# Optimization experiments

Hardware: AMD Instinct MI355X
Metric: run time of the kernel (lower is better)

## Reference

```python
import jax, jax.numpy as jnp
import numpy as np

EMB = 768
HEADS = 12
HEAD_DIM = EMB // HEADS  # 64
SCALE = 1.0 / float(np.sqrt(EMB))  # NOTE: source divides by sqrt(emb_size), not sqrt(head_dim)


def setup_inputs() -> dict:
    key = jax.random.key(0)
    k_x, k_wqkv, k_bqkv, k_wp, k_bp = jax.random.split(key, 5)
    b, n = 4, 2048
    x = jax.random.normal(k_x, (b, n, EMB), dtype=jnp.float32)
    # torch Linear default init ~ U(-1/sqrt(in), 1/sqrt(in)); scale doesn't matter for correctness baseline
    lim = 1.0 / np.sqrt(EMB)
    W_qkv = jax.random.uniform(k_wqkv, (EMB, 3 * EMB), minval=-lim, maxval=lim, dtype=jnp.float32)
    b_qkv = jax.random.uniform(k_bqkv, (3 * EMB,), minval=-lim, maxval=lim, dtype=jnp.float32)
    W_proj = jax.random.uniform(k_wp, (EMB, EMB), minval=-lim, maxval=lim, dtype=jnp.float32)
    b_proj = jax.random.uniform(k_bp, (EMB,), minval=-lim, maxval=lim, dtype=jnp.float32)
    return {"x": x, "W_qkv": W_qkv, "b_qkv": b_qkv, "W_proj": W_proj, "b_proj": b_proj}


def reference(x, W_qkv, b_qkv, W_proj, b_proj):
    b, n, _ = x.shape
    qkv = x @ W_qkv + b_qkv                              # [b, n, 3*emb]
    # rearrange 'b n (h d qkv) -> qkv b h n d' : qkv is the innermost split
    qkv = qkv.reshape(b, n, HEADS, HEAD_DIM, 3)
    qkv = jnp.transpose(qkv, (4, 0, 2, 1, 3))            # [3, b, h, n, d]
    q, k, v = qkv[0], qkv[1], qkv[2]
    att = jnp.einsum('bhnd,bhmd->bhnm', q, k) * SCALE    # [b, h, n, n]
    att = jax.nn.softmax(att, axis=-1)
    # dropout is identity at inference
    out = jnp.einsum('bhnm,bhmd->bhnd', att, v)          # [b, h, n, d]
    out = jnp.transpose(out, (0, 2, 1, 3)).reshape(b, n, EMB)  # 'b h n d -> b n (h d)'
    return out @ W_proj + b_proj
```

## Files before the change

### kernel.cpp

```cpp
#include <hip/hip_runtime.h>
#include <math.h>

typedef _Float16 f16x8 __attribute__((ext_vector_type(8)));
typedef _Float16 f16x4 __attribute__((ext_vector_type(4)));
typedef float f32x4 __attribute__((ext_vector_type(4)));
typedef unsigned int uint32;
typedef unsigned short ushort16;

static constexpr int EMB_ = 768;
static constexpr int NH_ = 12;
static constexpr int HD_ = 64;
static constexpr int SEQ_ = 2048;
static constexpr int B_ = 4;
static constexpr float QSCALE_ = 0.036084391824351615f * 1.4426950408889634f;

__device__ __forceinline__ void gload_lds16(const void* g, void* l) {
    __builtin_amdgcn_global_load_lds((const __attribute__((address_space(1))) void*)g,
                                     (__attribute__((address_space(3))) void*)l,
                                     16, 0, 0);
}

__global__ __launch_bounds__(256)
void prep_k(const float* __restrict__ W0, _Float16* __restrict__ Wt0,
            const float* __restrict__ W1, _Float16* __restrict__ Wt1,
            const float* __restrict__ x, _Float16* __restrict__ xh,
            int C0, int C1, int n4)
{
    const int tid = threadIdx.x;
    if (blockIdx.z == 2) {
        const int stride = 72 * 24 * 256;
        for (int i = (blockIdx.y * 72 + blockIdx.x) * 256 + tid; i < n4; i += stride) {
            float4 v = ((const float4*)x)[i];
            f16x4 o = {(_Float16)v.x, (_Float16)v.y, (_Float16)v.z, (_Float16)v.w};
            ((f16x4*)xh)[i] = o;
        }
        return;
    }
    const float* W; _Float16* Wt; int C;
    if (blockIdx.z == 0) { W = W0; Wt = Wt0; C = C0; }
    else                 { W = W1; Wt = Wt1; C = C1; }
    const int c0 = blockIdx.x * 32;
    if (c0 >= C) return;
    const int r0 = blockIdx.y * 32;
    __shared__ float ls[32][33];
    const int tc = tid & 31, tr = tid >> 5;
#pragma unroll
    for (int i = 0; i < 4; ++i)
        ls[tr + 8 * i][tc] = W[(size_t)(r0 + tr + 8 * i) * C + c0 + tc];
    __syncthreads();
#pragma unroll
    for (int i = 0; i < 4; ++i)
        Wt[(size_t)(c0 + tr + 8 * i) * EMB_ + r0 + tc] = (_Float16)ls[tc][tr + 8 * i];
}

template<int EPI>
__global__ __launch_bounds__(256, 2)
void gemm16(const _Float16* __restrict__ A, const _Float16* __restrict__ Bt,
            const float* __restrict__ bias, float* __restrict__ outF,
            _Float16* __restrict__ hq, _Float16* __restrict__ hk,
            _Float16* __restrict__ hv,
            int M, int N, int K)
{
    __shared__ __align__(16) _Float16 As[128 * 64];
    __shared__ __align__(16) _Float16 Bs[128 * 64];

    const int tid  = threadIdx.x;
    const int lane = tid & 63;
    const int w    = tid >> 6;
    const int txm  = lane & 15, g = lane >> 4;
    const int wr   = w >> 1, wc = w & 1;
    const int m0   = blockIdx.y * 128, n0 = blockIdx.x * 128;
    const int nk   = K >> 6;

    const int sr  = lane >> 3;
    const int scX = (((lane & 7) ^ sr) << 3);
    const _Float16* gA[4]; const _Float16* gB[4];
    _Float16* lA[4]; _Float16* lB[4];
#pragma unroll
    for (int i = 0; i < 4; ++i) {
        const int row = w * 32 + 8 * i;
        gA[i] = A  + (size_t)(m0 + row + sr) * K + scX;
        gB[i] = Bt + (size_t)(n0 + row + sr) * K + scX;
        lA[i] = As + row * 64 + lane * 8;
        lB[i] = Bs + row * 64 + lane * 8;
    }

    f32x4 acc[4][4];
#pragma unroll
    for (int i = 0; i < 4; ++i)
#pragma unroll
        for (int j = 0; j < 4; ++j) acc[i][j] = (f32x4){0.f, 0.f, 0.f, 0.f};

    const int fsw = txm & 7;

    for (int kt = 0; kt < nk; ++kt) {
        __syncthreads();
#pragma unroll
        for (int i = 0; i < 4; ++i) gload_lds16(gA[i] + kt * 64, lA[i]);
#pragma unroll
        for (int i = 0; i < 4; ++i) gload_lds16(gB[i] + kt * 64, lB[i]);
        __syncthreads();

#pragma unroll
        for (int kh = 0; kh < 2; ++kh) {
            const int coff = ((4 * kh + g) ^ fsw) << 3;
            f16x8 af[4], bf[4];
#pragma unroll
            for (int i = 0; i < 4; ++i)
                af[i] = *(const f16x8*)&As[(wr * 64 + 16 * i + txm) * 64 + coff];
#pragma unroll
            for (int j = 0; j < 4; ++j)
                bf[j] = *(const f16x8*)&Bs[(wc * 64 + 16 * j + txm) * 64 + coff];
#pragma unroll
            for (int i = 0; i < 4; ++i)
#pragma unroll
                for (int j = 0; j < 4; ++j)
                    acc[i][j] = __builtin_amdgcn_mfma_f32_16x16x32_f16(af[i], bf[j], acc[i][j], 0, 0, 0);
        }
    }

    if (EPI == 0) {
#pragma unroll
        for (int i = 0; i < 4; ++i) {
            const int mB = m0 + wr * 64 + 16 * i + 4 * g;
#pragma unroll
            for (int j = 0; j < 4; ++j) {
                const int n = n0 + wc * 64 + 16 * j + txm;
                const float bv = bias[n];
                const int h   = n / 192;
                const int rem = n - h * 192;
                const int dd  = rem / 3;
                const int s   = rem - dd * 3;
                _Float16* bse = (s == 0) ? hq : (s == 1) ? hk : hv;
                const float scl = (s == 0) ? QSCALE_ : 1.f;
#pragma unroll
                for (int r = 0; r < 4; ++r) {
                    const int mm = mB + r;
                    const int bb = mm >> 11;
                    const int nn = mm & (SEQ_ - 1);
                    const int ddE = (s == 1) ? (dd ^ ((nn & 7) * 8)) : dd;
                    bse[(((size_t)(bb * NH_ + h)) * SEQ_ + nn) * HD_ + ddE] =
                        (_Float16)((acc[i][j][r] + bv) * scl);
                }
            }
        }
    } else {
#pragma unroll
        for (int i = 0; i < 4; ++i) {
#pragma unroll
            for (int r = 0; r < 4; ++r) {
                const int mm = m0 + wr * 64 + 16 * i + 4 * g + r;
                float* dst = outF + (size_t)mm * N + n0 + wc * 64 + txm;
#pragma unroll
                for (int j = 0; j < 4; ++j)
                    dst[16 * j] = acc[i][j][r] + bias[n0 + wc * 64 + 16 * j + txm];
            }
        }
    }
}

__global__ __launch_bounds__(256, 3)
void attn_k(const _Float16* __restrict__ Qb, const _Float16* __restrict__ Kb,
            const _Float16* __restrict__ Vb, _Float16* __restrict__ Out)
{
    __shared__ __align__(16) _Float16 Ks[2][64][64];
    __shared__ __align__(16) _Float16 Vs[2][64][72];

    const int tid  = threadIdx.x;
    const int lane = tid & 63;
    const int wv   = tid >> 6;
    const int txm  = lane & 15;
    const int g    = lane >> 4;

    const int lin  = blockIdx.x;
    const int slot = lin >> 3;
    const int bh   = (lin & 7) + 8 * (slot >> 4);
    const int q0   = (slot & 15) << 7;
    const int bb   = bh / NH_;
    const int hh   = bh - bb * NH_;

    const _Float16* KpB = Kb + (size_t)bh * SEQ_ * HD_;
    const _Float16* VpB = Vb + (size_t)bh * SEQ_ * HD_;

    auto kstage = [&](int buf, int kt) {
        const int c0 = kt << 6;
#pragma unroll
        for (int i = 0; i < 2; ++i)
            gload_lds16(KpB + (size_t)(c0 + 16 * wv + 8 * i) * HD_ + lane * 8,
                        &Ks[buf][16 * wv + 8 * i][0] + lane * 8);
    };
    kstage(0, 0);

    f16x8 qf[2][2];
#pragma unroll
    for (int s = 0; s < 2; ++s)
#pragma unroll
        for (int kh = 0; kh < 2; ++kh)
            qf[s][kh] = *(const f16x8*)(Qb +
                ((size_t)bh * SEQ_ + q0 + 32 * wv + 16 * s + txm) * HD_ + 32 * kh + 8 * g);

    const int vc = (tid & 31) << 1;
    const int vd = (tid >> 5) << 3;
    const int swz = (txm & 7) * 8;

    f32x4 o[2][4];
#pragma unroll
    for (int s = 0; s < 2; ++s)
#pragma unroll
        for (int dt = 0; dt < 4; ++dt) o[s][dt] = (f32x4){0.f, 0.f, 0.f, 0.f};
    float li[2] = {0.f, 0.f};

    uint4 va = *(const uint4*)(VpB + (size_t)vc * HD_ + vd);
    uint4 vb = *(const uint4*)(VpB + (size_t)(vc + 1) * HD_ + vd);

    constexpr int NT = SEQ_ / 64;
    for (int kt = 0; kt < NT; ++kt) {
        const int buf = kt & 1;
        {
            const ushort16* pa = (const ushort16*)&va;
            const ushort16* pb = (const ushort16*)&vb;
#pragma unroll
            for (int j = 0; j < 8; ++j) {
                uint32 wrd = (uint32)pa[j] | ((uint32)pb[j] << 16);
                *(uint32*)&Vs[buf][vd + j][vc] = wrd;
            }
        }
        __syncthreads();

        if (kt + 1 < NT) {
            kstage(buf ^ 1, kt + 1);
            const int c0n = (kt + 1) << 6;
            va = *(const uint4*)(VpB + (size_t)(c0n + vc) * HD_ + vd);
            vb = *(const uint4*)(VpB + (size_t)(c0n + vc + 1) * HD_ + vd);
        }

        f16x8 kf[4][2];
#pragma unroll
        for (int ct = 0; ct < 4; ++ct)
#pragma unroll
            for (int kh = 0; kh < 2; ++kh)
                kf[ct][kh] = *(const f16x8*)&Ks[buf][16 * ct + txm][(32 * kh + 8 * g) ^ swz];

        f32x4 st[2][4];
#pragma unroll
        for (int s = 0; s < 2; ++s)
#pragma unroll
            for (int ct = 0; ct < 4; ++ct) {
                f32x4 a = (f32x4){0.f, 0.f, 0.f, 0.f};
                a = __builtin_amdgcn_mfma_f32_16x16x32_f16(kf[ct][0], qf[s][0], a, 0, 0, 0);
                a = __builtin_amdgcn_mfma_f32_16x16x32_f16(kf[ct][1], qf[s][1], a, 0, 0, 0);
                st[s][ct] = a;
            }

        f16x4 vf[4][4];
#pragma unroll
        for (int dt = 0; dt < 4; ++dt)
#pragma unroll
            for (int ct = 0; ct < 4; ++ct)
                vf[dt][ct] = *(const f16x4*)&Vs[buf][16 * dt + txm][16 * ct + 4 * g];

#pragma unroll
        for (int s = 0; s < 2; ++s) {
            f16x4 pb4[4];
#pragma unroll
            for (int ct = 0; ct < 4; ++ct) {
                float p0 = __builtin_amdgcn_exp2f(st[s][ct][0]);
                float p1 = __builtin_amdgcn_exp2f(st[s][ct][1]);
                float p2 = __builtin_amdgcn_exp2f(st[s][ct][2]);
                float p3 = __builtin_amdgcn_exp2f(st[s][ct][3]);
                li[s] += (p0 + p1) + (p2 + p3);
                pb4[ct] = (f16x4){(_Float16)p0, (_Float16)p1, (_Float16)p2, (_Float16)p3};
            }
#pragma unroll
            for (int dt = 0; dt < 4; ++dt) {
                f32x4 a = o[s][dt];
#pragma unroll
                for (int ct = 0; ct < 4; ++ct)
                    a = __builtin_amdgcn_mfma_f32_16x16x16f16(vf[dt][ct], pb4[ct], a, 0, 0, 0);
                o[s][dt] = a;
            }
        }
    }

#pragma unroll
    for (int s = 0; s < 2; ++s) {
        float rs = li[s];
        rs += __shfl_xor(rs, 16);
        rs += __shfl_xor(rs, 32);
        const float inv = 1.f / rs;
        const int q = q0 + 32 * wv + 16 * s + txm;
        _Float16* dst = Out + ((size_t)bb * SEQ_ + q) * EMB_ + hh * HD_;
#pragma unroll
        for (int dt = 0; dt < 4; ++dt) {
            f16x4 pk = {(_Float16)(o[s][dt][0] * inv), (_Float16)(o[s][dt][1] * inv),
                        (_Float16)(o[s][dt][2] * inv), (_Float16)(o[s][dt][3] * inv)};
            *(f16x4*)(dst + 16 * dt + 4 * g) = pk;
        }
    }
}

extern "C" void kernel_launch(void* const* d_in, const int* in_sizes, int n_in,
                              void* d_out, int out_size, void* d_ws, size_t ws_size,
                              hipStream_t stream)
{
    const float* x    = (const float*)d_in[0];
    const float* Wqkv = (const float*)d_in[1];
    const float* bqkv = (const float*)d_in[2];
    const float* Wp   = (const float*)d_in[3];
    const float* bp   = (const float*)d_in[4];
    float* out = (float*)d_out;

    const size_t PER = (size_t)B_ * NH_ * SEQ_ * HD_;
    _Float16* Qh     = (_Float16*)d_ws;
    _Float16* Kh     = Qh + PER;
    _Float16* Vh     = Kh + PER;
    _Float16* xh     = Vh + PER;
    _Float16* WqkvT  = xh + (size_t)B_ * SEQ_ * EMB_;
    _Float16* WprojT = WqkvT + (size_t)EMB_ * 3 * EMB_;
    _Float16* Ah     = WprojT + (size_t)EMB_ * EMB_;

    const int M = B_ * SEQ_;

    prep_k<<<dim3(72, 24, 3), dim3(256), 0, stream>>>(
        Wqkv, WqkvT, Wp, WprojT, x, xh, 3 * EMB_, EMB_, B_ * SEQ_ * EMB_ / 4);

    gemm16<0><<<dim3(3 * EMB_ / 128, M / 128), dim3(256), 0, stream>>>(
        xh, WqkvT, bqkv, nullptr, Qh, Kh, Vh, M, 3 * EMB_, EMB_);

    attn_k<<<dim3((SEQ_ / 128) * B_ * NH_), dim3(256), 0, stream>>>(Qh, Kh, Vh, Ah);

    gemm16<1><<<dim3(EMB_ / 128, M / 128), dim3(256), 0, stream>>>(
        Ah, WprojT, bp, out, nullptr, nullptr, nullptr, M, EMB_, EMB_);
}
```

Before: 233.0 us.

## Double-buffer GEMM LDS tiles and remap blocks to a grouped 1D grid

The fp16 GEMM kernel now keeps two LDS buffers per operand and issues the global-to-LDS loads for the next K tile before computing on the current one. This removes one barrier per iteration and lets load latency overlap with the MFMA work. The launch also becomes a 1D grid whose block index is remapped so groups of 8 consecutive blocks share an N tile across adjacent M tiles, which is meant to improve L2 reuse of the weight operand. LDS use per block doubles to 64 KB, which could limit occupancy. Only the QKV and output-projection GEMMs change; the attention kernel, which is likely the larger share of runtime, is untouched.

```diff
diff --git a/kernel.cpp b/kernel.cpp
--- a/kernel.cpp
+++ b/kernel.cpp
@@ -61,29 +61,40 @@
             _Float16* __restrict__ hv,
             int M, int N, int K)
 {
-    __shared__ __align__(16) _Float16 As[128 * 64];
-    __shared__ __align__(16) _Float16 Bs[128 * 64];
+    __shared__ __align__(16) _Float16 As[2][128 * 64];
+    __shared__ __align__(16) _Float16 Bs[2][128 * 64];
 
     const int tid  = threadIdx.x;
     const int lane = tid & 63;
     const int w    = tid >> 6;
     const int txm  = lane & 15, g = lane >> 4;
     const int wr   = w >> 1, wc = w & 1;
-    const int m0   = blockIdx.y * 128, n0 = blockIdx.x * 128;
+
+    const int lin  = blockIdx.x;
+    const int slot = lin >> 3;
+    const int mt   = (lin & 7) + 8 * (slot & 7);
+    const int nt   = slot >> 3;
+    const int m0   = mt * 128, n0 = nt * 128;
     const int nk   = K >> 6;
 
     const int sr  = lane >> 3;
     const int scX = (((lane & 7) ^ sr) << 3);
     const _Float16* gA[4]; const _Float16* gB[4];
-    _Float16* lA[4]; _Float16* lB[4];
 #pragma unroll
     for (int i = 0; i < 4; ++i) {
         const int row = w * 32 + 8 * i;
         gA[i] = A  + (size_t)(m0 + row + sr) * K + scX;
         gB[i] = Bt + (size_t)(n0 + row + sr) * K + scX;
-        lA[i] = As + row * 64 + lane * 8;
-        lB[i] = Bs + row * 64 + lane * 8;
-    }
+    }
+
+    auto stage = [&](int buf, int kt) {
+#pragma unroll
+        for (int i = 0; i < 4; ++i) {
+            const int row = w * 32 + 8 * i;
+            gload_lds16(gA[i] + kt * 64, &As[buf][row * 64] + lane * 8);
+            gload_lds16(gB[i] + kt * 64, &Bs[buf][row * 64] + lane * 8);
+        }
+    };
 
     f32x4 acc[4][4];
 #pragma unroll
@@ -93,13 +104,12 @@
 
     const int fsw = txm & 7;
 
+    stage(0, 0);
+
     for (int kt = 0; kt < nk; ++kt) {
+        const int buf = kt & 1;
         __syncthreads();
-#pragma unroll
-        for (int i = 0; i < 4; ++i) gload_lds16(gA[i] + kt * 64, lA[i]);
-#pragma unroll
-        for (int i = 0; i < 4; ++i) gload_lds16(gB[i] + kt * 64, lB[i]);
-        __syncthreads();
+        if (kt + 1 < nk) stage(buf ^ 1, kt + 1);
 
 #pragma unroll
         for (int kh = 0; kh < 2; ++kh) {
@@ -107,10 +117,10 @@
             f16x8 af[4], bf[4];
 #pragma unroll
             for (int i = 0; i < 4; ++i)
-                af[i] = *(const f16x8*)&As[(wr * 64 + 16 * i + txm) * 64 + coff];
+                af[i] = *(const f16x8*)&As[buf][(wr * 64 + 16 * i + txm) * 64 + coff];
 #pragma unroll
             for (int j = 0; j < 4; ++j)
-                bf[j] = *(const f16x8*)&Bs[(wc * 64 + 16 * j + txm) * 64 + coff];
+                bf[j] = *(const f16x8*)&Bs[buf][(wc * 64 + 16 * j + txm) * 64 + coff];
 #pragma unroll
             for (int i = 0; i < 4; ++i)
 #pragma unroll
@@ -324,11 +334,11 @@
     prep_k<<<dim3(72, 24, 3), dim3(256), 0, stream>>>(
         Wqkv, WqkvT, Wp, WprojT, x, xh, 3 * EMB_, EMB_, B_ * SEQ_ * EMB_ / 4);
 
-    gemm16<0><<<dim3(3 * EMB_ / 128, M / 128), dim3(256), 0, stream>>>(
+    gemm16<0><<<dim3((M / 128) * (3 * EMB_ / 128)), dim3(256), 0, stream>>>(
         xh, WqkvT, bqkv, nullptr, Qh, Kh, Vh, M, 3 * EMB_, EMB_);
 
     attn_k<<<dim3((SEQ_ / 128) * B_ * NH_), dim3(256), 0, stream>>>(Qh, Kh, Vh, Ah);
 
-    gemm16<1><<<dim3(EMB_ / 128, M / 128), dim3(256), 0, stream>>>(
+    gemm16<1><<<dim3((M / 128) * (EMB_ / 128)), dim3(256), 0, stream>>>(
         Ah, WprojT, bp, out, nullptr, nullptr, nullptr, M, EMB_, EMB_);
 }
```

New measurement: 237.5 us. Within noise of the previous version (+1.9%).
